# Kernel tuning notes

Hardware: AMD Instinct MI355X
Metric: run time of the kernel (lower is better)

## Reference

```python
import jax, jax.numpy as jnp
import numpy as np

B, S, D = 4, 1024, 1024
H = 16
HD = D // H  # 64
LN_EPS = 1e-5


def setup_inputs() -> dict:
    key = jax.random.key(0)
    ks = jax.random.split(key, 12)
    s = 1.0 / np.sqrt(D)
    return {
        "x": jax.random.normal(ks[0], (B, S, D), dtype=jnp.float32),
        "wq": jax.random.normal(ks[1], (D, D), dtype=jnp.float32) * s,
        "bq": jnp.zeros((D,), dtype=jnp.float32),
        "wk": jax.random.normal(ks[2], (D, D), dtype=jnp.float32) * s,
        "bk": jnp.zeros((D,), dtype=jnp.float32),
        "wv": jax.random.normal(ks[3], (D, D), dtype=jnp.float32) * s,
        "bv": jnp.zeros((D,), dtype=jnp.float32),
        "wl": jax.random.normal(ks[4], (D, D), dtype=jnp.float32) * s,
        "bl": jnp.zeros((D,), dtype=jnp.float32),
        "ln_g": jnp.ones((D,), dtype=jnp.float32),
        "ln_b": jnp.zeros((D,), dtype=jnp.float32),
    }


def _heads(t):
    # [B,S,D] -> [B,H,S,HD]
    return t.reshape(B, S, H, HD).transpose(0, 2, 1, 3)


def reference(x, wq, bq, wk, bk, wv, bv, wl, bl, ln_g, ln_b):
    q = _heads(x @ wq.T + bq)
    k = _heads(x @ wk.T + bk)
    v = _heads(x @ wv.T + bv)
    score = jnp.einsum("bhqd,bhkd->bhqk", q, k)
    # NOTE: unusual order — softmax first, THEN divide by sqrt(head_size)
    score = jax.nn.softmax(score, axis=-1) / jnp.sqrt(jnp.float32(HD))
    att = jnp.einsum("bhqk,bhkd->bhqd", score, v)
    att = att.transpose(0, 2, 1, 3).reshape(B, S, D)
    # residual added BEFORE the output linear
    y = (att + x) @ wl.T + bl
    # LayerNorm over last dim
    mu = jnp.mean(y, axis=-1, keepdims=True)
    var = jnp.mean(jnp.square(y - mu), axis=-1, keepdims=True)
    out = (y - mu) * jax.lax.rsqrt(var + LN_EPS) * ln_g + ln_b
    # dropout is identity in eval mode
    return out
```

## Files before the change

kernel.cpp:

```cpp
#include <hip/hip_runtime.h>
#include <cstdint>
#include <cstddef>

typedef __bf16 bf16;
typedef __bf16 bf16x4_t __attribute__((ext_vector_type(4)));
typedef __bf16 bf16x8_t __attribute__((ext_vector_type(8)));
typedef float f32x4_t __attribute__((ext_vector_type(4)));

#define DEV static __device__ __forceinline__

DEV void gload16(const void* g, void* l) {
  __builtin_amdgcn_global_load_lds((const __attribute__((address_space(1))) void*)g,
                                   (__attribute__((address_space(3))) void*)l, 16, 0, 0);
}

DEV f32x4_t mfma16(bf16x8_t a, bf16x8_t b, f32x4_t c) {
  return __builtin_amdgcn_mfma_f32_16x16x32_bf16(a, b, c, 0, 0, 0);
}

#define BAR __builtin_amdgcn_s_barrier()
#define FENCE asm volatile("" ::: "memory")
#define LGKM0 do { asm volatile("s_waitcnt lgkmcnt(0)" ::: "memory"); \
                   __builtin_amdgcn_sched_barrier(0); } while (0)
#define VMC(n) asm volatile("s_waitcnt vmcnt(" #n ")" ::: "memory")

__global__ __launch_bounds__(256) void k_convert(
    const float* __restrict__ x, const float* __restrict__ wq,
    const float* __restrict__ wk, const float* __restrict__ wv,
    const float* __restrict__ wl,
    bf16* __restrict__ xb, bf16* __restrict__ wqkvb, bf16* __restrict__ wlb) {
  const size_t M1 = (size_t)1 << 20;
  size_t i = ((size_t)blockIdx.x * 256 + threadIdx.x) * 4;
  const float* src; bf16* dst; size_t off;
  if (i < 4 * M1)      { src = x;  dst = xb;           off = i; }
  else if (i < 5 * M1) { src = wq; dst = wqkvb;        off = i - 4 * M1; }
  else if (i < 6 * M1) { src = wk; dst = wqkvb + M1;   off = i - 5 * M1; }
  else if (i < 7 * M1) { src = wv; dst = wqkvb + 2*M1; off = i - 6 * M1; }
  else                 { src = wl; dst = wlb;          off = i - 7 * M1; }
  f32x4_t v = *(const f32x4_t*)&src[off];
  bf16x4_t o;
  o[0] = (bf16)v[0]; o[1] = (bf16)v[1]; o[2] = (bf16)v[2]; o[3] = (bf16)v[3];
  *(bf16x4_t*)&dst[off] = o;
}

__global__ __launch_bounds__(512, 2) void k_gemm_qkv(
    const bf16* __restrict__ W, const bf16* __restrict__ Xb,
    const float* __restrict__ bq, const float* __restrict__ bk,
    const float* __restrict__ bv,
    bf16* __restrict__ Q, bf16* __restrict__ Kc, bf16* __restrict__ VT) {
  __shared__ alignas(16) bf16 lA[2][256 * 64];
  __shared__ alignas(16) bf16 lB[2][256 * 64];
  const int tid = threadIdx.x, w = tid >> 6, lane = tid & 63;
  const int wr = w >> 2, wc = w & 3;
  const int fr = lane & 15, fg = lane >> 4;
  const int srow = lane >> 3;
  const int csw = (((lane & 7) ^ srow) << 3);
  const int m0 = blockIdx.x * 256, n0 = blockIdx.y * 256;

  f32x4_t acc[8][4];
  const f32x4_t vzero = {0.f, 0.f, 0.f, 0.f};
#pragma unroll
  for (int a = 0; a < 8; ++a)
#pragma unroll
    for (int c = 0; c < 4; ++c) acc[a][c] = vzero;

  auto SA = [&](int buf, int kt, int row0) {
    gload16(W + (size_t)(m0 + row0 + srow) * 1024 + kt * 64 + csw,
            &lA[buf][row0 * 64]);
  };
  auto SB = [&](int buf, int kt, int row0) {
    gload16(Xb + (size_t)(n0 + row0 + srow) * 1024 + kt * 64 + csw,
            &lB[buf][row0 * 64]);
  };
  const int a0 = w * 8;
  const int b0 = (w >> 2) * 64 + (w & 3) * 8;

  bf16x8_t af[4][2], bfr[4][2];

  auto LDA = [&](int buf, int qm) {
#pragma unroll
    for (int mi = 0; mi < 4; ++mi)
#pragma unroll
      for (int ks = 0; ks < 2; ++ks) {
        const int r = wr * 128 + qm * 64 + mi * 16 + fr;
        af[mi][ks] = *(const bf16x8_t*)
            &lA[buf][r * 64 + ((((ks << 2) + fg) ^ (r & 7)) << 3)];
      }
  };
  auto LDB = [&](int buf, int qn) {
#pragma unroll
    for (int i = 0; i < 2; ++i)
#pragma unroll
      for (int ks = 0; ks < 2; ++ks) {
        const int r = wc * 64 + (qn * 2 + i) * 16 + fr;
        bfr[qn * 2 + i][ks] = *(const bf16x8_t*)
            &lB[buf][r * 64 + ((((ks << 2) + fg) ^ (r & 7)) << 3)];
      }
  };
  auto MM = [&](int qm, int qn) {
    __builtin_amdgcn_s_setprio(1);
#pragma unroll
    for (int ks = 0; ks < 2; ++ks)
#pragma unroll
      for (int mi = 0; mi < 4; ++mi)
#pragma unroll
        for (int i = 0; i < 2; ++i)
          acc[qm * 4 + mi][qn * 2 + i] =
              mfma16(af[mi][ks], bfr[qn * 2 + i][ks], acc[qm * 4 + mi][qn * 2 + i]);
    __builtin_amdgcn_s_setprio(0);
  };

  SA(0, 0, a0); SA(0, 0, a0 + 64); SA(0, 0, a0 + 128); SA(0, 0, a0 + 192);
  SB(0, 0, a0); SB(0, 0, a0 + 64); SB(0, 0, a0 + 128); SB(0, 0, a0 + 192);
  SA(1, 1, a0); SA(1, 1, a0 + 128);
  SB(1, 1, b0); SB(1, 1, b0 + 128);
  SB(1, 1, b0 + 32); SB(1, 1, b0 + 160);
  VMC(6); BAR; FENCE;

#pragma unroll 2
  for (int t = 0; t < 14; ++t) {
    const int p = t & 1;
    LDA(p, 0); LDB(p, 0);
    SA(p ^ 1, t + 1, a0 + 64); SA(p ^ 1, t + 1, a0 + 192);
    BAR; FENCE; LGKM0;
    MM(0, 0);
    BAR; FENCE;
    LDB(p, 1);
    SA(p, t + 2, a0); SA(p, t + 2, a0 + 128);
    BAR; FENCE; LGKM0;
    MM(0, 1);
    BAR; FENCE;
    LDA(p, 1);
    SB(p, t + 2, b0); SB(p, t + 2, b0 + 128);
    BAR; FENCE; LGKM0;
    MM(1, 0);
    BAR; FENCE;
    SB(p, t + 2, b0 + 32); SB(p, t + 2, b0 + 160);
    BAR; FENCE;
    MM(1, 1);
    VMC(6);
    BAR; FENCE;
  }
  {
    LDA(0, 0); LDB(0, 0);
    SA(1, 15, a0 + 64); SA(1, 15, a0 + 192);
    BAR; FENCE; LGKM0; MM(0, 0); BAR; FENCE;
    LDB(0, 1);
    BAR; FENCE; LGKM0; MM(0, 1); BAR; FENCE;
    LDA(0, 1);
    BAR; FENCE; LGKM0; MM(1, 0); BAR; FENCE;
    MM(1, 1);
    VMC(0);
    BAR; FENCE;
  }
  {
    LDA(1, 0); LDB(1, 0);
    BAR; FENCE; LGKM0; MM(0, 0); BAR; FENCE;
    LDB(1, 1);
    BAR; FENCE; LGKM0; MM(0, 1); BAR; FENCE;
    LDA(1, 1);
    BAR; FENCE; LGKM0; MM(1, 0); BAR; FENCE;
    MM(1, 1);
  }

  const int region = m0 >> 10;
  const float* bp = (region == 0) ? bq : ((region == 1) ? bk : bv);
  bf16* QK = (region == 0) ? Q : Kc;
#pragma unroll
  for (int mi = 0; mi < 8; ++mi) {
    const int f = (m0 & 1023) + wr * 128 + mi * 16 + fg * 4;
    const int h = f >> 6, d = f & 63;
#pragma unroll
    for (int ni = 0; ni < 4; ++ni) {
      const int tkn = n0 + wc * 64 + ni * 16 + fr;
      const int b = tkn >> 10, s = tkn & 1023;
      const int bh = b * 16 + h;
      f32x4_t v = acc[mi][ni];
      if (region < 2) {
        bf16x4_t o;
#pragma unroll
        for (int j = 0; j < 4; ++j) o[j] = (bf16)(v[j] + bp[f + j]);
        *(bf16x4_t*)&QK[((size_t)bh * 1024 + s) * 64 + d] = o;
      } else {
#pragma unroll
        for (int j = 0; j < 4; ++j)
          VT[((size_t)bh * 64 + d + j) * 1024 + s] = (bf16)(v[j] + bp[f + j]);
      }
    }
  }
}

DEV void gemm_mainloop(const bf16* __restrict__ A, const bf16* __restrict__ B,
                       int m0, int n0,
                       bf16 (*lA)[128 * 64], bf16 (*lB)[128 * 64],
                       f32x4_t (&acc)[4][4]) {
  const int tid = threadIdx.x, wave = tid >> 6, lane = tid & 63;
  const int wm = (wave >> 1) * 64, wn = (wave & 1) * 64;
  const int fr = lane & 15, fg = lane >> 4;
  const int rowoff = wave * 8 + (lane >> 3);
  const int csw = (((lane & 7) ^ (lane >> 3)) << 3);

  auto STAGE = [&](int buf, int kt) {
#pragma unroll
    for (int i = 0; i < 4; ++i) {
      gload16(A + (size_t)(m0 + i * 32 + rowoff) * 1024 + kt * 64 + csw,
              &lA[buf][(i * 32 + wave * 8) * 64]);
      gload16(B + (size_t)(n0 + i * 32 + rowoff) * 1024 + kt * 64 + csw,
              &lB[buf][(i * 32 + wave * 8) * 64]);
    }
  };

  auto COMPUTE = [&](int buf) {
    bf16x8_t af[4][2], bfr[4][2];
#pragma unroll
    for (int mi = 0; mi < 4; ++mi)
#pragma unroll
      for (int ks = 0; ks < 2; ++ks) {
        const int r = wm + mi * 16 + fr;
        af[mi][ks] = *(const bf16x8_t*)
            &lA[buf][r * 64 + ((((ks << 2) + fg) ^ (fr & 7)) << 3)];
      }
#pragma unroll
    for (int ni = 0; ni < 4; ++ni)
#pragma unroll
      for (int ks = 0; ks < 2; ++ks) {
        const int r = wn + ni * 16 + fr;
        bfr[ni][ks] = *(const bf16x8_t*)
            &lB[buf][r * 64 + ((((ks << 2) + fg) ^ (fr & 7)) << 3)];
      }
    __builtin_amdgcn_s_setprio(1);
#pragma unroll
    for (int ks = 0; ks < 2; ++ks)
#pragma unroll
      for (int mi = 0; mi < 4; ++mi)
#pragma unroll
        for (int ni = 0; ni < 4; ++ni)
          acc[mi][ni] = mfma16(af[mi][ks], bfr[ni][ks], acc[mi][ni]);
    __builtin_amdgcn_s_setprio(0);
  };

  STAGE(0, 0);
  STAGE(1, 1);
  for (int t = 0; t < 15; ++t) {
    asm volatile("s_waitcnt vmcnt(8)" ::: "memory");
    __builtin_amdgcn_s_barrier();
    COMPUTE(t & 1);
    __builtin_amdgcn_s_barrier();
    if (t < 14) STAGE(t & 1, t + 2);
  }
  asm volatile("s_waitcnt vmcnt(0)" ::: "memory");
  __builtin_amdgcn_s_barrier();
  COMPUTE(1);
}

#define P_STRIDE 72

__global__ __launch_bounds__(256) void k_attn(
    const bf16* __restrict__ Q, const bf16* __restrict__ K,
    const bf16* __restrict__ VT, const float* __restrict__ X,
    bf16* __restrict__ ATTB) {
  __shared__ alignas(16) bf16 lK[2][64 * 64];
  __shared__ alignas(16) bf16 lV[2][64 * 64];
  __shared__ alignas(16) bf16 lP[4][32 * P_STRIDE];
  const int tid = threadIdx.x, wave = tid >> 6, lane = tid & 63;
  const int bh = blockIdx.x, qt = blockIdx.y;
  const int q0 = qt * 128 + wave * 32;
  const int fr = lane & 15, fg = lane >> 4;
  const int rx = (fr & 7) << 3;
  const f32x4_t vzero = {0.f, 0.f, 0.f, 0.f};

  bf16x8_t qf[2][2];
#pragma unroll
  for (int mi = 0; mi < 2; ++mi)
#pragma unroll
    for (int ks = 0; ks < 2; ++ks)
      qf[mi][ks] = *(const bf16x8_t*)
          &Q[((size_t)bh * 1024 + q0 + mi * 16 + fr) * 64 + ks * 32 + fg * 8];

  f32x4_t oacc[2][4];
  f32x4_t lsum[2];
#pragma unroll
  for (int mi = 0; mi < 2; ++mi) {
    lsum[mi] = vzero;
#pragma unroll
    for (int dj = 0; dj < 4; ++dj) oacc[mi][dj] = vzero;
  }

  const int srow = lane >> 3;
  const int scolsw = (((lane & 7) ^ srow) * 8);

  auto STAGE = [&](int buf, int kv) {
#pragma unroll
    for (int i = 0; i < 2; ++i) {
      const int c = wave * 2 + i;
      gload16(&K[((size_t)bh * 1024 + kv * 64 + c * 8 + srow) * 64 + scolsw],
              &lK[buf][c * 512]);
      gload16(&VT[((size_t)bh * 64 + c * 8 + srow) * 1024 + kv * 64 + scolsw],
              &lV[buf][c * 512]);
    }
  };

  STAGE(0, 0);
  __syncthreads();

  for (int kv = 0; kv < 16; ++kv) {
    const int cur = kv & 1;
    if (kv < 15) STAGE(cur ^ 1, kv + 1);

    bf16x8_t kb[4][2];
#pragma unroll
    for (int nj = 0; nj < 4; ++nj)
#pragma unroll
      for (int ks = 0; ks < 2; ++ks) {
        const int r = nj * 16 + fr;
        kb[nj][ks] = *(const bf16x8_t*)&lK[cur][r * 64 + ((ks * 32 + fg * 8) ^ rx)];
      }
    f32x4_t s[2][4];
#pragma unroll
    for (int mi = 0; mi < 2; ++mi)
#pragma unroll
      for (int nj = 0; nj < 4; ++nj) {
        f32x4_t z = vzero;
#pragma unroll
        for (int ks = 0; ks < 2; ++ks) z = mfma16(qf[mi][ks], kb[nj][ks], z);
        s[mi][nj] = z;
      }

#pragma unroll
    for (int mi = 0; mi < 2; ++mi)
#pragma unroll
      for (int nj = 0; nj < 4; ++nj)
#pragma unroll
        for (int j = 0; j < 4; ++j) {
          float p = __expf(s[mi][nj][j]);
          lsum[mi][j] += p;
          lP[wave][(mi * 16 + fg * 4 + j) * P_STRIDE + nj * 16 + fr] = (bf16)p;
        }

    bf16x8_t vb[4][2], pa[2][2];
#pragma unroll
    for (int dj = 0; dj < 4; ++dj)
#pragma unroll
      for (int ks = 0; ks < 2; ++ks) {
        const int r = dj * 16 + fr;
        vb[dj][ks] = *(const bf16x8_t*)&lV[cur][r * 64 + ((ks * 32 + fg * 8) ^ rx)];
      }
#pragma unroll
    for (int mi = 0; mi < 2; ++mi)
#pragma unroll
      for (int ks = 0; ks < 2; ++ks)
        pa[mi][ks] = *(const bf16x8_t*)
            &lP[wave][(mi * 16 + fr) * P_STRIDE + ks * 32 + fg * 8];
#pragma unroll
    for (int mi = 0; mi < 2; ++mi)
#pragma unroll
      for (int dj = 0; dj < 4; ++dj)
#pragma unroll
        for (int ks = 0; ks < 2; ++ks)
          oacc[mi][dj] = mfma16(pa[mi][ks], vb[dj][ks], oacc[mi][dj]);

    __syncthreads();
  }

#pragma unroll
  for (int mi = 0; mi < 2; ++mi)
#pragma unroll
    for (int m = 1; m < 16; m <<= 1)
#pragma unroll
      for (int j = 0; j < 4; ++j)
        lsum[mi][j] += __shfl_xor(lsum[mi][j], m);

  const int b = bh >> 4, h = bh & 15;
#pragma unroll
  for (int mi = 0; mi < 2; ++mi)
#pragma unroll
    for (int dj = 0; dj < 4; ++dj)
#pragma unroll
      for (int j = 0; j < 4; ++j) {
        const int s_ = q0 + mi * 16 + fg * 4 + j;
        const int d_ = dj * 16 + fr;
        const size_t tok = (size_t)b * 1024 + s_;
        const size_t fidx = (size_t)h * 64 + d_;
        float val = oacc[mi][dj][j] / lsum[mi][j] * 0.125f + X[tok * 1024 + fidx];
        ATTB[tok * 1024 + fidx] = (bf16)val;
      }
}

__global__ __launch_bounds__(256, 2) void k_gemm_out(
    const bf16* __restrict__ Wl, const bf16* __restrict__ Ax,
    const float* __restrict__ bl, float* __restrict__ Y) {
  __shared__ alignas(16) bf16 lA[2][128 * 64];
  __shared__ alignas(16) bf16 lB[2][128 * 64];
  const f32x4_t vzero = {0.f, 0.f, 0.f, 0.f};
  f32x4_t acc[4][4];
#pragma unroll
  for (int a = 0; a < 4; ++a)
#pragma unroll
    for (int c = 0; c < 4; ++c) acc[a][c] = vzero;
  const int m0 = blockIdx.x * 128, n0 = blockIdx.y * 128;
  gemm_mainloop(Wl, Ax, m0, n0, lA, lB, acc);

  const int tid = threadIdx.x, wave = tid >> 6, lane = tid & 63;
  const int wm = (wave >> 1) * 64, wn = (wave & 1) * 64;
  const int fr = lane & 15, fg = lane >> 4;
#pragma unroll
  for (int mi = 0; mi < 4; ++mi) {
    const int f = m0 + wm + mi * 16 + fg * 4;
#pragma unroll
    for (int ni = 0; ni < 4; ++ni) {
      const int t = n0 + wn + ni * 16 + fr;
      f32x4_t v = acc[mi][ni], o;
#pragma unroll
      for (int j = 0; j < 4; ++j) o[j] = v[j] + bl[f + j];
      *(f32x4_t*)&Y[(size_t)t * 1024 + f] = o;
    }
  }
}

__global__ __launch_bounds__(256) void k_ln(
    const float* __restrict__ Y, const float* __restrict__ g,
    const float* __restrict__ bta, float* __restrict__ OUT) {
  const int row = blockIdx.x, tid = threadIdx.x;
  const float* y = Y + (size_t)row * 1024;
  f32x4_t v = *(const f32x4_t*)&y[tid * 4];
  float s = v[0] + v[1] + v[2] + v[3];
  float s2 = v[0]*v[0] + v[1]*v[1] + v[2]*v[2] + v[3]*v[3];
#pragma unroll
  for (int m = 1; m < 64; m <<= 1) {
    s += __shfl_xor(s, m);
    s2 += __shfl_xor(s2, m);
  }
  __shared__ float ps[4], ps2[4];
  const int wave = tid >> 6, lane = tid & 63;
  if (lane == 0) { ps[wave] = s; ps2[wave] = s2; }
  __syncthreads();
  s = ps[0] + ps[1] + ps[2] + ps[3];
  s2 = ps2[0] + ps2[1] + ps2[2] + ps2[3];
  const float mu = s * (1.f / 1024.f);
  const float var = s2 * (1.f / 1024.f) - mu * mu;
  const float rs = rsqrtf(var + 1e-5f);
  f32x4_t gg = *(const f32x4_t*)&g[tid * 4];
  f32x4_t bb = *(const f32x4_t*)&bta[tid * 4];
  f32x4_t o;
#pragma unroll
  for (int j = 0; j < 4; ++j) o[j] = (v[j] - mu) * rs * gg[j] + bb[j];
  *(f32x4_t*)&OUT[(size_t)row * 1024 + tid * 4] = o;
}

extern "C" void kernel_launch(void* const* d_in, const int* in_sizes, int n_in,
                              void* d_out, int out_size, void* d_ws, size_t ws_size,
                              hipStream_t stream) {
  (void)in_sizes; (void)n_in; (void)out_size; (void)ws_size;
  const float* x   = (const float*)d_in[0];
  const float* wq  = (const float*)d_in[1];
  const float* bq  = (const float*)d_in[2];
  const float* wk  = (const float*)d_in[3];
  const float* bk  = (const float*)d_in[4];
  const float* wv  = (const float*)d_in[5];
  const float* bv  = (const float*)d_in[6];
  const float* wl  = (const float*)d_in[7];
  const float* bl  = (const float*)d_in[8];
  const float* lng = (const float*)d_in[9];
  const float* lnb = (const float*)d_in[10];

  const size_t MB = (size_t)1 << 20;
  char* ws = (char*)d_ws;
  bf16* xb    = (bf16*)(ws);
  bf16* wqkvb = (bf16*)(ws + 8 * MB);
  bf16* wlb   = (bf16*)(ws + 14 * MB);
  bf16* Qb    = (bf16*)(ws + 16 * MB);
  bf16* Kb    = (bf16*)(ws + 24 * MB);
  bf16* VTb   = (bf16*)(ws + 32 * MB);
  bf16* attb  = (bf16*)(ws + 40 * MB);
  float* Y    = (float*)(ws + 16 * MB);

  k_convert<<<dim3(8192), dim3(256), 0, stream>>>(x, wq, wk, wv, wl, xb, wqkvb, wlb);
  k_gemm_qkv<<<dim3(12, 16), dim3(512), 0, stream>>>(wqkvb, xb, bq, bk, bv, Qb, Kb, VTb);
  k_attn<<<dim3(64, 8), dim3(256), 0, stream>>>(Qb, Kb, VTb, x, attb);
  k_gemm_out<<<dim3(8, 32), dim3(256), 0, stream>>>(wlb, attb, bl, Y);
  k_ln<<<dim3(4096), dim3(256), 0, stream>>>(Y, lng, lnb, (float*)d_out);
}
```

Baseline: 111.9 us.

## Retile QKV GEMM to 192-row tiles and prefetch attention K/V two ahead

The QKV projection GEMM switches from 256x256 to 192x256 tiles, so the grid grows from 192 to 256 blocks, matching the CU count more closely. The K loop is reorganised into three A sub-phases with one B fragment load, and the explicit lgkmcnt waits are dropped. The epilogue now computes the Q/K/V region per fragment, because one tile can span two regions. The attention kernel now keeps two K/V tiles in flight and waits with vmcnt instead of a full syncthreads, which adds LDS-pressure and sync-correctness risk. Removing LGKM0 relies on the compiler inserting the LDS waits.

```diff
diff --git a/kernel.cpp b/kernel.cpp
--- a/kernel.cpp
+++ b/kernel.cpp
@@ -20,8 +20,6 @@
 
 #define BAR __builtin_amdgcn_s_barrier()
 #define FENCE asm volatile("" ::: "memory")
-#define LGKM0 do { asm volatile("s_waitcnt lgkmcnt(0)" ::: "memory"); \
-                   __builtin_amdgcn_sched_barrier(0); } while (0)
 #define VMC(n) asm volatile("s_waitcnt vmcnt(" #n ")" ::: "memory")
 
 __global__ __launch_bounds__(256) void k_convert(
@@ -48,21 +46,22 @@
     const float* __restrict__ bq, const float* __restrict__ bk,
     const float* __restrict__ bv,
     bf16* __restrict__ Q, bf16* __restrict__ Kc, bf16* __restrict__ VT) {
-  __shared__ alignas(16) bf16 lA[2][256 * 64];
+  __shared__ alignas(16) bf16 lA[2][192 * 64];
   __shared__ alignas(16) bf16 lB[2][256 * 64];
   const int tid = threadIdx.x, w = tid >> 6, lane = tid & 63;
   const int wr = w >> 2, wc = w & 3;
   const int fr = lane & 15, fg = lane >> 4;
   const int srow = lane >> 3;
   const int csw = (((lane & 7) ^ srow) << 3);
-  const int m0 = blockIdx.x * 256, n0 = blockIdx.y * 256;
-
-  f32x4_t acc[8][4];
+  const int m0 = blockIdx.x * 192, n0 = blockIdx.y * 256;
+  const int a = w * 8;
+
+  f32x4_t acc[6][4];
   const f32x4_t vzero = {0.f, 0.f, 0.f, 0.f};
 #pragma unroll
-  for (int a = 0; a < 8; ++a)
-#pragma unroll
-    for (int c = 0; c < 4; ++c) acc[a][c] = vzero;
+  for (int i = 0; i < 6; ++i)
+#pragma unroll
+    for (int c = 0; c < 4; ++c) acc[i][c] = vzero;
 
   auto SA = [&](int buf, int kt, int row0) {
     gload16(W + (size_t)(m0 + row0 + srow) * 1024 + kt * 64 + csw,
@@ -72,104 +71,93 @@
     gload16(Xb + (size_t)(n0 + row0 + srow) * 1024 + kt * 64 + csw,
             &lB[buf][row0 * 64]);
   };
-  const int a0 = w * 8;
-  const int b0 = (w >> 2) * 64 + (w & 3) * 8;
-
-  bf16x8_t af[4][2], bfr[4][2];
-
+
+  bf16x8_t af[2][2], bfr[4][2];
   auto LDA = [&](int buf, int qm) {
 #pragma unroll
-    for (int mi = 0; mi < 4; ++mi)
-#pragma unroll
-      for (int ks = 0; ks < 2; ++ks) {
-        const int r = wr * 128 + qm * 64 + mi * 16 + fr;
+    for (int mi = 0; mi < 2; ++mi)
+#pragma unroll
+      for (int ks = 0; ks < 2; ++ks) {
+        const int r = wr * 96 + qm * 32 + mi * 16 + fr;
         af[mi][ks] = *(const bf16x8_t*)
-            &lA[buf][r * 64 + ((((ks << 2) + fg) ^ (r & 7)) << 3)];
-      }
-  };
-  auto LDB = [&](int buf, int qn) {
-#pragma unroll
-    for (int i = 0; i < 2; ++i)
-#pragma unroll
-      for (int ks = 0; ks < 2; ++ks) {
-        const int r = wc * 64 + (qn * 2 + i) * 16 + fr;
-        bfr[qn * 2 + i][ks] = *(const bf16x8_t*)
-            &lB[buf][r * 64 + ((((ks << 2) + fg) ^ (r & 7)) << 3)];
-      }
-  };
-  auto MM = [&](int qm, int qn) {
+            &lA[buf][r * 64 + ((((ks << 2) + fg) ^ (fr & 7)) << 3)];
+      }
+  };
+  auto LDB = [&](int buf) {
+#pragma unroll
+    for (int ni = 0; ni < 4; ++ni)
+#pragma unroll
+      for (int ks = 0; ks < 2; ++ks) {
+        const int r = wc * 64 + ni * 16 + fr;
+        bfr[ni][ks] = *(const bf16x8_t*)
+            &lB[buf][r * 64 + ((((ks << 2) + fg) ^ (fr & 7)) << 3)];
+      }
+  };
+  auto MM = [&](int qm) {
     __builtin_amdgcn_s_setprio(1);
 #pragma unroll
     for (int ks = 0; ks < 2; ++ks)
 #pragma unroll
-      for (int mi = 0; mi < 4; ++mi)
-#pragma unroll
-        for (int i = 0; i < 2; ++i)
-          acc[qm * 4 + mi][qn * 2 + i] =
-              mfma16(af[mi][ks], bfr[qn * 2 + i][ks], acc[qm * 4 + mi][qn * 2 + i]);
+      for (int mi = 0; mi < 2; ++mi)
+#pragma unroll
+        for (int ni = 0; ni < 4; ++ni)
+          acc[qm * 2 + mi][ni] =
+              mfma16(af[mi][ks], bfr[ni][ks], acc[qm * 2 + mi][ni]);
     __builtin_amdgcn_s_setprio(0);
   };
 
-  SA(0, 0, a0); SA(0, 0, a0 + 64); SA(0, 0, a0 + 128); SA(0, 0, a0 + 192);
-  SB(0, 0, a0); SB(0, 0, a0 + 64); SB(0, 0, a0 + 128); SB(0, 0, a0 + 192);
-  SA(1, 1, a0); SA(1, 1, a0 + 128);
-  SB(1, 1, b0); SB(1, 1, b0 + 128);
-  SB(1, 1, b0 + 32); SB(1, 1, b0 + 160);
-  VMC(6); BAR; FENCE;
+  SA(0, 0, a); SA(0, 0, a + 64); SA(0, 0, a + 128);
+  SB(0, 0, a); SB(0, 0, a + 64); SB(0, 0, a + 128); SB(0, 0, a + 192);
+  SB(1, 1, a); SB(1, 1, a + 64); SB(1, 1, a + 128); SB(1, 1, a + 192);
+  SA(1, 1, a);
+  VMC(5); BAR; FENCE;
 
 #pragma unroll 2
   for (int t = 0; t < 14; ++t) {
     const int p = t & 1;
-    LDA(p, 0); LDB(p, 0);
-    SA(p ^ 1, t + 1, a0 + 64); SA(p ^ 1, t + 1, a0 + 192);
-    BAR; FENCE; LGKM0;
-    MM(0, 0);
-    BAR; FENCE;
-    LDB(p, 1);
-    SA(p, t + 2, a0); SA(p, t + 2, a0 + 128);
-    BAR; FENCE; LGKM0;
-    MM(0, 1);
+    LDA(p, 0); LDB(p);
+    SA(p ^ 1, t + 1, a + 64); SA(p ^ 1, t + 1, a + 128);
+    BAR; FENCE;
+    MM(0);
     BAR; FENCE;
     LDA(p, 1);
-    SB(p, t + 2, b0); SB(p, t + 2, b0 + 128);
-    BAR; FENCE; LGKM0;
-    MM(1, 0);
-    BAR; FENCE;
-    SB(p, t + 2, b0 + 32); SB(p, t + 2, b0 + 160);
-    BAR; FENCE;
-    MM(1, 1);
-    VMC(6);
+    SB(p, t + 2, a); SB(p, t + 2, a + 64);
+    SB(p, t + 2, a + 128); SB(p, t + 2, a + 192);
+    BAR; FENCE;
+    MM(1);
+    BAR; FENCE;
+    LDA(p, 2);
+    SA(p, t + 2, a);
+    BAR; FENCE;
+    MM(2);
+    VMC(5);
     BAR; FENCE;
   }
   {
-    LDA(0, 0); LDB(0, 0);
-    SA(1, 15, a0 + 64); SA(1, 15, a0 + 192);
-    BAR; FENCE; LGKM0; MM(0, 0); BAR; FENCE;
-    LDB(0, 1);
-    BAR; FENCE; LGKM0; MM(0, 1); BAR; FENCE;
+    LDA(0, 0); LDB(0);
+    SA(1, 15, a + 64); SA(1, 15, a + 128);
+    BAR; FENCE; MM(0); BAR; FENCE;
     LDA(0, 1);
-    BAR; FENCE; LGKM0; MM(1, 0); BAR; FENCE;
-    MM(1, 1);
-    VMC(0);
-    BAR; FENCE;
+    BAR; FENCE; MM(1); BAR; FENCE;
+    LDA(0, 2);
+    BAR; FENCE; MM(2);
+    VMC(0); BAR; FENCE;
   }
   {
-    LDA(1, 0); LDB(1, 0);
-    BAR; FENCE; LGKM0; MM(0, 0); BAR; FENCE;
-    LDB(1, 1);
-    BAR; FENCE; LGKM0; MM(0, 1); BAR; FENCE;
-    LDA(1, 1);
-    BAR; FENCE; LGKM0; MM(1, 0); BAR; FENCE;
-    MM(1, 1);
-  }
-
-  const int region = m0 >> 10;
-  const float* bp = (region == 0) ? bq : ((region == 1) ? bk : bv);
-  bf16* QK = (region == 0) ? Q : Kc;
-#pragma unroll
-  for (int mi = 0; mi < 8; ++mi) {
-    const int f = (m0 & 1023) + wr * 128 + mi * 16 + fg * 4;
-    const int h = f >> 6, d = f & 63;
+    LDA(1, 0); LDB(1);
+    MM(0);
+    LDA(1, 1); MM(1);
+    LDA(1, 2); MM(2);
+  }
+
+#pragma unroll
+  for (int mi = 0; mi < 6; ++mi) {
+    const int f = m0 + wr * 96 + mi * 16 + fg * 4;
+    const int region = f >> 10;
+    const int floc = f & 1023;
+    const int h = floc >> 6, d = floc & 63;
+    const float* bp = (region == 0) ? bq : ((region == 1) ? bk : bv);
+    bf16* QK = (region == 0) ? Q : Kc;
 #pragma unroll
     for (int ni = 0; ni < 4; ++ni) {
       const int tkn = n0 + wc * 64 + ni * 16 + fr;
@@ -179,12 +167,12 @@
       if (region < 2) {
         bf16x4_t o;
 #pragma unroll
-        for (int j = 0; j < 4; ++j) o[j] = (bf16)(v[j] + bp[f + j]);
+        for (int j = 0; j < 4; ++j) o[j] = (bf16)(v[j] + bp[floc + j]);
         *(bf16x4_t*)&QK[((size_t)bh * 1024 + s) * 64 + d] = o;
       } else {
 #pragma unroll
         for (int j = 0; j < 4; ++j)
-          VT[((size_t)bh * 64 + d + j) * 1024 + s] = (bf16)(v[j] + bp[f + j]);
+          VT[((size_t)bh * 64 + d + j) * 1024 + s] = (bf16)(v[j] + bp[floc + j]);
       }
     }
   }
@@ -300,13 +288,7 @@
     }
   };
 
-  STAGE(0, 0);
-  __syncthreads();
-
-  for (int kv = 0; kv < 16; ++kv) {
-    const int cur = kv & 1;
-    if (kv < 15) STAGE(cur ^ 1, kv + 1);
-
+  auto TILE = [&](int cur) {
     bf16x8_t kb[4][2];
 #pragma unroll
     for (int nj = 0; nj < 4; ++nj)
@@ -358,9 +340,18 @@
 #pragma unroll
         for (int ks = 0; ks < 2; ++ks)
           oacc[mi][dj] = mfma16(pa[mi][ks], vb[dj][ks], oacc[mi][dj]);
-
-    __syncthreads();
-  }
+  };
+
+  STAGE(0, 0);
+  STAGE(1, 1);
+  for (int kv = 0; kv < 15; ++kv) {
+    VMC(4); BAR; FENCE;
+    TILE(kv & 1);
+    BAR; FENCE;
+    if (kv < 14) STAGE(kv & 1, kv + 2);
+  }
+  VMC(0); BAR; FENCE;
+  TILE(1);
 
 #pragma unroll
   for (int mi = 0; mi < 2; ++mi)
@@ -475,7 +466,7 @@
   float* Y    = (float*)(ws + 16 * MB);
 
   k_convert<<<dim3(8192), dim3(256), 0, stream>>>(x, wq, wk, wv, wl, xb, wqkvb, wlb);
-  k_gemm_qkv<<<dim3(12, 16), dim3(512), 0, stream>>>(wqkvb, xb, bq, bk, bv, Qb, Kb, VTb);
+  k_gemm_qkv<<<dim3(16, 16), dim3(512), 0, stream>>>(wqkvb, xb, bq, bk, bv, Qb, Kb, VTb);
   k_attn<<<dim3(64, 8), dim3(256), 0, stream>>>(Qb, Kb, VTb, x, attb);
   k_gemm_out<<<dim3(8, 32), dim3(256), 0, stream>>>(wlb, attb, bl, Y);
   k_ln<<<dim3(4096), dim3(256), 0, stream>>>(Y, lng, lnb, (float*)d_out);
```

Result: no change. 110.8 us (-1.0%).
